# Performance work log

Hardware: AMD Instinct MI355X
Metric: run time of the kernel (lower is better)

## Reference

```python
import jax, jax.numpy as jnp
import numpy as np

B, N, D_IN = 4, 16384, 64          # batch, sequence (grid) length, model dim
H, DH = 8, 64                       # heads, dim per head
INNER = H * DH                      # 512


def setup_inputs() -> dict:
    key = jax.random.key(0)
    ks = jax.random.split(key, 7)
    s = 1.0 / np.sqrt(D_IN)
    return {
        "queries": jax.random.normal(ks[0], (B, N, D_IN), jnp.float32),
        "keys": jax.random.normal(ks[1], (B, N, D_IN), jnp.float32),
        "values": jax.random.normal(ks[2], (B, N, D_IN), jnp.float32),
        # torch nn.Linear weights are [out_features, in_features]
        "Wq": jax.random.normal(ks[3], (INNER, D_IN), jnp.float32) * s,
        "Wk": jax.random.normal(ks[4], (INNER, D_IN), jnp.float32) * s,
        "Wout": jax.random.normal(ks[5], (D_IN, INNER), jnp.float32) * (1.0 / np.sqrt(INNER)),
        "bout": jax.random.normal(ks[6], (D_IN,), jnp.float32) * 0.01,
    }


def reference(queries, keys, values, Wq, Wk, Wout, bout):
    b, n, _ = queries.shape
    # projections (NOTE: source uses to_k for values: values = self.to_k(values))
    q = (queries @ Wq.T).reshape(b, n, H, DH).transpose(0, 2, 1, 3)  # b h n d
    k = (keys    @ Wk.T).reshape(b, n, H, DH).transpose(0, 2, 1, 3)
    v = (values  @ Wk.T).reshape(b, n, H, DH).transpose(0, 2, 1, 3)
    # galerkin linear attention, associative form: (K^T V) first, then Q @ (.)
    # (the instance-norm outputs in the torch source are dead code on this path)
    dots = jnp.einsum('bhnd,bhne->bhde', k, v)            # [b,h,d,d]
    out = jnp.einsum('bhnd,bhde->bhne', q, dots) / n      # [b,h,n,d]
    out = out.transpose(0, 2, 1, 3).reshape(b, n, INNER)  # b n (h d)
    return out @ Wout.T + bout                             # [b,n,D_IN]
```

## Files before the change

kernel.cpp:

```cpp
#include <hip/hip_runtime.h>

#define NB 4
#define SEQ 16384
#define D 64
#define NH 8
#define INNER 512

constexpr int S_RPB  = 256;
constexpr int S_TILE = 32;

__global__ __launch_bounds__(256) void k_S(const float* __restrict__ keys,
                                           const float* __restrict__ values,
                                           float* __restrict__ S) {
    __shared__ float ks[S_TILE][D];
    __shared__ float vs[S_TILE][D];
    const int b = blockIdx.y;
    const int t = threadIdx.x;
    const size_t base = ((size_t)b * SEQ + (size_t)blockIdx.x * S_RPB) * D;
    const float4* ksrc = (const float4*)(keys + base);
    const float4* vsrc = (const float4*)(values + base);
    const int di = t >> 4;
    const int ej = t & 15;
    float acc[4][4] = {{0.f}};
    for (int tile = 0; tile < S_RPB / S_TILE; ++tile) {
        float4* kd = (float4*)&ks[0][0];
        float4* vd = (float4*)&vs[0][0];
        const int off = tile * (S_TILE * D / 4);
        kd[t]       = ksrc[off + t];
        kd[t + 256] = ksrc[off + t + 256];
        vd[t]       = vsrc[off + t];
        vd[t + 256] = vsrc[off + t + 256];
        __syncthreads();
        #pragma unroll 8
        for (int n = 0; n < S_TILE; ++n) {
            float kv[4], vv[4];
            #pragma unroll
            for (int a = 0; a < 4; ++a) kv[a] = ks[n][di + 16 * a];
            #pragma unroll
            for (int c = 0; c < 4; ++c) vv[c] = vs[n][ej + 16 * c];
            #pragma unroll
            for (int a = 0; a < 4; ++a)
                #pragma unroll
                for (int c = 0; c < 4; ++c)
                    acc[a][c] = fmaf(kv[a], vv[c], acc[a][c]);
        }
        __syncthreads();
    }
    float* Sb = S + b * D * D;
    #pragma unroll
    for (int a = 0; a < 4; ++a)
        #pragma unroll
        for (int c = 0; c < 4; ++c)
            atomicAdd(&Sb[(di + 16 * a) * D + (ej + 16 * c)], acc[a][c]);
}

__global__ __launch_bounds__(256) void k_G(const float* __restrict__ S,
                                           const float* __restrict__ Wq,
                                           const float* __restrict__ Wk,
                                           const float* __restrict__ Wout,
                                           float* __restrict__ G) {
    __shared__ float Ss[D][D];
    __shared__ float W1[D][D];
    __shared__ float T1[D][D];
    __shared__ float T2[D][D];
    const int b = blockIdx.x >> 3;
    const int h = blockIdx.x & 7;
    const int t = threadIdx.x;
    const int di = t >> 4, ej = t & 15;

    const float* Sb  = S + b * D * D;
    const float* Wkh = Wk + h * D * D;
    for (int i = t; i < D * D; i += 256) {
        (&Ss[0][0])[i] = Sb[i];
        (&W1[0][0])[i] = Wkh[i];
    }
    __syncthreads();

    float acc[4][4];

    #pragma unroll
    for (int a = 0; a < 4; ++a)
        #pragma unroll
        for (int c = 0; c < 4; ++c) acc[a][c] = 0.f;
    for (int i = 0; i < D; ++i) {
        float wa[4], sv[4];
        #pragma unroll
        for (int a = 0; a < 4; ++a) wa[a] = W1[di + 16 * a][i];
        #pragma unroll
        for (int c = 0; c < 4; ++c) sv[c] = Ss[i][ej + 16 * c];
        #pragma unroll
        for (int a = 0; a < 4; ++a)
            #pragma unroll
            for (int c = 0; c < 4; ++c) acc[a][c] = fmaf(wa[a], sv[c], acc[a][c]);
    }
    #pragma unroll
    for (int a = 0; a < 4; ++a)
        #pragma unroll
        for (int c = 0; c < 4; ++c) T1[di + 16 * a][ej + 16 * c] = acc[a][c];
    __syncthreads();

    #pragma unroll
    for (int a = 0; a < 4; ++a)
        #pragma unroll
        for (int c = 0; c < 4; ++c) acc[a][c] = 0.f;
    for (int i = 0; i < D; ++i) {
        float ta[4], wb[4];
        #pragma unroll
        for (int a = 0; a < 4; ++a) ta[a] = T1[di + 16 * a][i];
        #pragma unroll
        for (int c = 0; c < 4; ++c) wb[c] = W1[ej + 16 * c][i];
        #pragma unroll
        for (int a = 0; a < 4; ++a)
            #pragma unroll
            for (int c = 0; c < 4; ++c) acc[a][c] = fmaf(ta[a], wb[c], acc[a][c]);
    }
    #pragma unroll
    for (int a = 0; a < 4; ++a)
        #pragma unroll
        for (int c = 0; c < 4; ++c) T2[di + 16 * a][ej + 16 * c] = acc[a][c];
    __syncthreads();

    const float* Wqh = Wq + h * D * D;
    for (int i = t; i < D * D; i += 256) (&W1[0][0])[i] = Wqh[i];
    __syncthreads();

    #pragma unroll
    for (int a = 0; a < 4; ++a)
        #pragma unroll
        for (int c = 0; c < 4; ++c) acc[a][c] = 0.f;
    for (int i = 0; i < D; ++i) {
        float wa[4], tb[4];
        #pragma unroll
        for (int a = 0; a < 4; ++a) wa[a] = W1[i][di + 16 * a];
        #pragma unroll
        for (int c = 0; c < 4; ++c) tb[c] = T2[i][ej + 16 * c];
        #pragma unroll
        for (int a = 0; a < 4; ++a)
            #pragma unroll
            for (int c = 0; c < 4; ++c) acc[a][c] = fmaf(wa[a], tb[c], acc[a][c]);
    }
    #pragma unroll
    for (int a = 0; a < 4; ++a)
        #pragma unroll
        for (int c = 0; c < 4; ++c) T1[di + 16 * a][ej + 16 * c] = acc[a][c];
    __syncthreads();

    for (int i = t; i < D * D; i += 256) {
        int r = i >> 6, c2 = i & 63;
        (&W1[0][0])[i] = Wout[r * INNER + h * D + c2];
    }
    __syncthreads();

    #pragma unroll
    for (int a = 0; a < 4; ++a)
        #pragma unroll
        for (int c = 0; c < 4; ++c) acc[a][c] = 0.f;
    for (int i = 0; i < D; ++i) {
        float ta[4], wb[4];
        #pragma unroll
        for (int a = 0; a < 4; ++a) ta[a] = T1[di + 16 * a][i];
        #pragma unroll
        for (int c = 0; c < 4; ++c) wb[c] = W1[ej + 16 * c][i];
        #pragma unroll
        for (int a = 0; a < 4; ++a)
            #pragma unroll
            for (int c = 0; c < 4; ++c) acc[a][c] = fmaf(ta[a], wb[c], acc[a][c]);
    }
    const float invn = 1.0f / (float)SEQ;
    float* Gb = G + b * D * D;
    #pragma unroll
    for (int a = 0; a < 4; ++a)
        #pragma unroll
        for (int c = 0; c < 4; ++c)
            atomicAdd(&Gb[(di + 16 * a) * D + (ej + 16 * c)], acc[a][c] * invn);
}

constexpr int A_ROWS = 64;

__global__ __launch_bounds__(256) void k_apply(const float* __restrict__ queries,
                                               const float* __restrict__ G,
                                               const float* __restrict__ bout,
                                               float* __restrict__ out) {
    __shared__ float Gs[D][D];
    __shared__ float qs[A_ROWS][D + 4];
    const int b = blockIdx.y;
    const int t = threadIdx.x;
    const size_t base = ((size_t)b * SEQ + (size_t)blockIdx.x * A_ROWS) * D;
    const float4* qsrc = (const float4*)(queries + base);
    const float4* Gsrc = (const float4*)(G + b * D * D);
    float4* Gd = (float4*)&Gs[0][0];
    #pragma unroll
    for (int i = 0; i < 4; ++i) {
        const int idx = t + 256 * i;
        Gd[idx] = Gsrc[idx];
        float4 qv = qsrc[idx];
        const int r = idx >> 4;
        const int c = (idx & 15) * 4;
        *(float4*)&qs[r][c] = qv;
    }
    __syncthreads();

    const int d4 = (t & 15) * 4;
    const int rg = t >> 4;
    const float4 bo = *(const float4*)&bout[d4];
    float acc[4][4] = {{0.f}};
    #pragma unroll 8
    for (int i = 0; i < D; ++i) {
        const float4 g = *(const float4*)&Gs[i][d4];
        #pragma unroll
        for (int r = 0; r < 4; ++r) {
            const float qv = qs[rg + 16 * r][i];
            acc[r][0] = fmaf(qv, g.x, acc[r][0]);
            acc[r][1] = fmaf(qv, g.y, acc[r][1]);
            acc[r][2] = fmaf(qv, g.z, acc[r][2]);
            acc[r][3] = fmaf(qv, g.w, acc[r][3]);
        }
    }
    float* ob = out + base;
    #pragma unroll
    for (int r = 0; r < 4; ++r) {
        float4 o = make_float4(acc[r][0] + bo.x, acc[r][1] + bo.y,
                               acc[r][2] + bo.z, acc[r][3] + bo.w);
        *(float4*)&ob[(rg + 16 * r) * D + d4] = o;
    }
}

extern "C" void kernel_launch(void* const* d_in, const int* in_sizes, int n_in,
                              void* d_out, int out_size, void* d_ws, size_t ws_size,
                              hipStream_t stream) {
    const float* queries = (const float*)d_in[0];
    const float* keys    = (const float*)d_in[1];
    const float* values  = (const float*)d_in[2];
    const float* Wq      = (const float*)d_in[3];
    const float* Wk      = (const float*)d_in[4];
    const float* Wout    = (const float*)d_in[5];
    const float* bout    = (const float*)d_in[6];
    float* out = (float*)d_out;

    float* S = (float*)d_ws;
    float* G = S + NB * D * D;
    hipMemsetAsync(d_ws, 0, (size_t)2 * NB * D * D * sizeof(float), stream);

    k_S<<<dim3(SEQ / S_RPB, NB), 256, 0, stream>>>(keys, values, S);
    k_G<<<NB * NH, 256, 0, stream>>>(S, Wq, Wk, Wout, G);
    k_apply<<<dim3(SEQ / A_ROWS, NB), 256, 0, stream>>>(queries, G, bout, out);
}
```

Measured before the change: 152.5 us.

## Restructure pipeline into five kernels with weight-product precompute and atomic-free reduction

The three kernels are replaced by five. kA computes per-block partial K^T V tiles with no atomics and, in the same launch, the per-head weight products Wq^T Wk and Wout Wk. kB reduces the partials, and kC/kD fold the reduced matrix and the weight products into G using a different association, so only a small atomic reduction over head chunks remains. kE applies G to the queries using a transposed, XOR-swizzled copy of G in shared memory while reading queries straight from global memory. The aim is to remove the heavy atomic contention and the serial per-head matmul chain, at the cost of more launches and extra workspace traffic.

```diff
diff --git a/kernel.cpp b/kernel.cpp
--- a/kernel.cpp
+++ b/kernel.cpp
@@ -6,222 +6,253 @@
 #define NH 8
 #define INNER 512
 
-constexpr int S_RPB  = 256;
-constexpr int S_TILE = 32;
-
-__global__ __launch_bounds__(256) void k_S(const float* __restrict__ keys,
-                                           const float* __restrict__ values,
-                                           float* __restrict__ S) {
-    __shared__ float ks[S_TILE][D];
-    __shared__ float vs[S_TILE][D];
-    const int b = blockIdx.y;
-    const int t = threadIdx.x;
-    const size_t base = ((size_t)b * SEQ + (size_t)blockIdx.x * S_RPB) * D;
-    const float4* ksrc = (const float4*)(keys + base);
-    const float4* vsrc = (const float4*)(values + base);
-    const int di = t >> 4;
-    const int ej = t & 15;
-    float acc[4][4] = {{0.f}};
-    for (int tile = 0; tile < S_RPB / S_TILE; ++tile) {
-        float4* kd = (float4*)&ks[0][0];
-        float4* vd = (float4*)&vs[0][0];
-        const int off = tile * (S_TILE * D / 4);
-        kd[t]       = ksrc[off + t];
-        kd[t + 256] = ksrc[off + t + 256];
-        vd[t]       = vsrc[off + t];
-        vd[t + 256] = vsrc[off + t + 256];
-        __syncthreads();
-        #pragma unroll 8
-        for (int n = 0; n < S_TILE; ++n) {
-            float kv[4], vv[4];
-            #pragma unroll
-            for (int a = 0; a < 4; ++a) kv[a] = ks[n][di + 16 * a];
-            #pragma unroll
-            for (int c = 0; c < 4; ++c) vv[c] = vs[n][ej + 16 * c];
-            #pragma unroll
-            for (int a = 0; a < 4; ++a)
-                #pragma unroll
-                for (int c = 0; c < 4; ++c)
-                    acc[a][c] = fmaf(kv[a], vv[c], acc[a][c]);
-        }
-        __syncthreads();
-    }
-    float* Sb = S + b * D * D;
+typedef float f4 __attribute__((ext_vector_type(4)));
+
+#define OFF_PART 0
+#define OFF_S    (256 * 4096)
+#define OFF_P    (OFF_S + NB * 4096)
+#define OFF_Q    (OFF_P + 64 * INNER)
+#define OFF_XT   (OFF_Q + INNER * D)
+#define OFF_G    (OFF_XT + NB * 64 * INNER)
+
+__global__ __launch_bounds__(256) void kA(const float* __restrict__ keys,
+                                          const float* __restrict__ values,
+                                          const float* __restrict__ Wq,
+                                          const float* __restrict__ Wk,
+                                          const float* __restrict__ Wout,
+                                          float* __restrict__ ws) {
+    const int bid = blockIdx.x;
+    const int t = threadIdx.x;
+    const int w = t >> 6, l = t & 63;
+    const int dg = l >> 3, eg = l & 7;
+    const int dbase = (w & 1) * 32 + dg * 4;
+    const int ebase = (w >> 1) * 32 + eg * 4;
+
+    f4 acc[4];
+    #pragma unroll
+    for (int a = 0; a < 4; ++a) acc[a] = (f4)0.f;
+
+    if (bid < 256) {
+        const int b = bid >> 6;
+        const int row0 = (bid & 63) * 256;
+        const float* kp = keys   + ((size_t)b * SEQ + row0) * D;
+        const float* vp = values + ((size_t)b * SEQ + row0) * D;
+        #pragma unroll 4
+        for (int n = 0; n < 256; ++n) {
+            f4 kv = *(const f4*)(kp + n * D + dbase);
+            f4 vv = *(const f4*)(vp + n * D + ebase);
+            #pragma unroll
+            for (int a = 0; a < 4; ++a)
+                acc[a] += kv[a] * vv;
+        }
+        float* pp = ws + OFF_PART + (size_t)bid * 4096;
+        #pragma unroll
+        for (int a = 0; a < 4; ++a)
+            *(f4*)(pp + (dbase + a) * D + ebase) = acc[a];
+    } else if (bid < 264) {
+        const int h = bid - 256;
+        const float* wqp = Wq + (size_t)h * 64 * D;
+        const float* wkp = Wk + (size_t)h * 64 * D;
+        #pragma unroll 4
+        for (int i = 0; i < 64; ++i) {
+            f4 a4 = *(const f4*)(wqp + i * D + dbase);
+            f4 b4 = *(const f4*)(wkp + i * D + ebase);
+            #pragma unroll
+            for (int a = 0; a < 4; ++a)
+                acc[a] += a4[a] * b4;
+        }
+        float* pp = ws + OFF_P;
+        #pragma unroll
+        for (int a = 0; a < 4; ++a)
+            *(f4*)(pp + (dbase + a) * INNER + h * 64 + ebase) = acc[a];
+    } else {
+        const int h = bid - 264;
+        const float* wkp = Wk + (size_t)h * 64 * D;
+        #pragma unroll 2
+        for (int iq = 0; iq < 16; ++iq) {
+            f4 wo[4], wk4[4];
+            #pragma unroll
+            for (int a = 0; a < 4; ++a)
+                wo[a] = *(const f4*)(Wout + (size_t)(dbase + a) * INNER + h * 64 + iq * 4);
+            #pragma unroll
+            for (int ii = 0; ii < 4; ++ii)
+                wk4[ii] = *(const f4*)(wkp + (iq * 4 + ii) * D + ebase);
+            #pragma unroll
+            for (int a = 0; a < 4; ++a)
+                #pragma unroll
+                for (int ii = 0; ii < 4; ++ii)
+                    acc[a] += wo[a][ii] * wk4[ii];
+        }
+        float* qp = ws + OFF_Q;
+        #pragma unroll
+        for (int a = 0; a < 4; ++a)
+            *(f4*)(qp + (h * 64 + dbase + a) * D + ebase) = acc[a];
+    }
+}
+
+__global__ __launch_bounds__(256) void kB(float* __restrict__ ws) {
+    const int b = blockIdx.x >> 5;
+    const int seg = blockIdx.x & 31;
+    const int t = threadIdx.x;
+    const int el = seg * 128 + (t & 127);
+    const int half = t >> 7;
+    const float* pp = ws + OFF_PART + (size_t)b * 64 * 4096 + el;
+    float s = 0.f;
+    #pragma unroll 8
+    for (int p = 0; p < 32; ++p)
+        s += pp[(size_t)(half * 32 + p) * 4096];
+    __shared__ float red[256];
+    red[t] = s;
+    __syncthreads();
+    if (t < 128)
+        ws[OFF_S + b * 4096 + el] = red[t] + red[t + 128];
+}
+
+__global__ __launch_bounds__(256) void kC(float* __restrict__ ws) {
+    const int b = blockIdx.x >> 3, h = blockIdx.x & 7;
+    const int t = threadIdx.x;
+    if (h == 0) {
+        f4 z = (f4)0.f;
+        #pragma unroll
+        for (int m = 0; m < 4; ++m)
+            *(f4*)(ws + OFF_G + b * 4096 + t * 16 + m * 4) = z;
+    }
+    const int w = t >> 6, l = t & 63;
+    const int dbase = (w & 1) * 32 + (l >> 3) * 4;
+    const int ebase = (w >> 1) * 32 + (l & 7) * 4;
+    const float* Sp = ws + OFF_S + b * 4096;
+    const float* Qp = ws + OFF_Q + h * 64 * D;
+    float acc[4][4];
     #pragma unroll
     for (int a = 0; a < 4; ++a)
         #pragma unroll
+        for (int c = 0; c < 4; ++c) acc[a][c] = 0.f;
+    #pragma unroll 2
+    for (int iq = 0; iq < 16; ++iq) {
+        f4 s4[4], q4[4];
+        #pragma unroll
+        for (int a = 0; a < 4; ++a) s4[a] = *(const f4*)(Sp + (dbase + a) * D + iq * 4);
+        #pragma unroll
+        for (int c = 0; c < 4; ++c) q4[c] = *(const f4*)(Qp + (ebase + c) * D + iq * 4);
+        #pragma unroll
+        for (int a = 0; a < 4; ++a)
+            #pragma unroll
+            for (int c = 0; c < 4; ++c)
+                #pragma unroll
+                for (int ii = 0; ii < 4; ++ii)
+                    acc[a][c] = fmaf(s4[a][ii], q4[c][ii], acc[a][c]);
+    }
+    float* xp = ws + OFF_XT + (size_t)b * 64 * INNER;
+    #pragma unroll
+    for (int c = 0; c < 4; ++c) {
+        f4 o;
+        o[0] = acc[0][c]; o[1] = acc[1][c]; o[2] = acc[2][c]; o[3] = acc[3][c];
+        *(f4*)(xp + (size_t)(ebase + c) * INNER + h * 64 + dbase) = o;
+    }
+}
+
+__global__ __launch_bounds__(256) void kD(float* __restrict__ ws) {
+    const int b = blockIdx.x >> 4;
+    const int kc = (blockIdx.x & 15) * 32;
+    const int t = threadIdx.x;
+    const int w = t >> 6, l = t & 63;
+    const int dbase = (w & 1) * 32 + (l >> 3) * 4;
+    const int ebase = (w >> 1) * 32 + (l & 7) * 4;
+    const float* Pp = ws + OFF_P;
+    const float* Xp = ws + OFF_XT + (size_t)b * 64 * INNER;
+    float acc[4][4];
+    #pragma unroll
+    for (int a = 0; a < 4; ++a)
+        #pragma unroll
+        for (int c = 0; c < 4; ++c) acc[a][c] = 0.f;
+    #pragma unroll
+    for (int kq = 0; kq < 8; ++kq) {
+        f4 p4[4], x4[4];
+        #pragma unroll
+        for (int a = 0; a < 4; ++a) p4[a] = *(const f4*)(Pp + (size_t)(dbase + a) * INNER + kc + kq * 4);
+        #pragma unroll
+        for (int c = 0; c < 4; ++c) x4[c] = *(const f4*)(Xp + (size_t)(ebase + c) * INNER + kc + kq * 4);
+        #pragma unroll
+        for (int a = 0; a < 4; ++a)
+            #pragma unroll
+            for (int c = 0; c < 4; ++c)
+                #pragma unroll
+                for (int ii = 0; ii < 4; ++ii)
+                    acc[a][c] = fmaf(p4[a][ii], x4[c][ii], acc[a][c]);
+    }
+    const float invn = 1.0f / (float)SEQ;
+    float* Gp = ws + OFF_G + b * 4096;
+    #pragma unroll
+    for (int a = 0; a < 4; ++a)
+        #pragma unroll
         for (int c = 0; c < 4; ++c)
-            atomicAdd(&Sb[(di + 16 * a) * D + (ej + 16 * c)], acc[a][c]);
-}
-
-__global__ __launch_bounds__(256) void k_G(const float* __restrict__ S,
-                                           const float* __restrict__ Wq,
-                                           const float* __restrict__ Wk,
-                                           const float* __restrict__ Wout,
-                                           float* __restrict__ G) {
-    __shared__ float Ss[D][D];
-    __shared__ float W1[D][D];
-    __shared__ float T1[D][D];
-    __shared__ float T2[D][D];
-    const int b = blockIdx.x >> 3;
-    const int h = blockIdx.x & 7;
-    const int t = threadIdx.x;
-    const int di = t >> 4, ej = t & 15;
-
-    const float* Sb  = S + b * D * D;
-    const float* Wkh = Wk + h * D * D;
-    for (int i = t; i < D * D; i += 256) {
-        (&Ss[0][0])[i] = Sb[i];
-        (&W1[0][0])[i] = Wkh[i];
+            atomicAdd(&Gp[(dbase + a) * D + ebase + c], acc[a][c] * invn);
+}
+
+__global__ __launch_bounds__(256) void kE(const float* __restrict__ queries,
+                                          const float* __restrict__ bout,
+                                          const float* __restrict__ ws,
+                                          float* __restrict__ out) {
+    __shared__ float GTs[4096];
+    const int bid = blockIdx.x;
+    const int b = bid >> 6;
+    const int row0 = (bid & 63) * 256;
+    const int t = threadIdx.x;
+    {
+        const int d = t >> 2;
+        const int e0 = (t & 3) * 16;
+        #pragma unroll
+        for (int m4 = 0; m4 < 4; ++m4) {
+            f4 g = *(const f4*)(ws + OFF_G + b * 4096 + d * 64 + e0 + m4 * 4);
+            #pragma unroll
+            for (int mm = 0; mm < 4; ++mm) {
+                const int e = e0 + m4 * 4 + mm;
+                GTs[e * 64 + (((d >> 2) ^ ((e >> 3) & 7)) << 2) + (d & 3)] = g[mm];
+            }
+        }
     }
     __syncthreads();
 
-    float acc[4][4];
-
-    #pragma unroll
-    for (int a = 0; a < 4; ++a)
-        #pragma unroll
-        for (int c = 0; c < 4; ++c) acc[a][c] = 0.f;
-    for (int i = 0; i < D; ++i) {
-        float wa[4], sv[4];
-        #pragma unroll
-        for (int a = 0; a < 4; ++a) wa[a] = W1[di + 16 * a][i];
-        #pragma unroll
-        for (int c = 0; c < 4; ++c) sv[c] = Ss[i][ej + 16 * c];
-        #pragma unroll
-        for (int a = 0; a < 4; ++a)
-            #pragma unroll
-            for (int c = 0; c < 4; ++c) acc[a][c] = fmaf(wa[a], sv[c], acc[a][c]);
-    }
-    #pragma unroll
-    for (int a = 0; a < 4; ++a)
-        #pragma unroll
-        for (int c = 0; c < 4; ++c) T1[di + 16 * a][ej + 16 * c] = acc[a][c];
-    __syncthreads();
-
-    #pragma unroll
-    for (int a = 0; a < 4; ++a)
-        #pragma unroll
-        for (int c = 0; c < 4; ++c) acc[a][c] = 0.f;
-    for (int i = 0; i < D; ++i) {
-        float ta[4], wb[4];
-        #pragma unroll
-        for (int a = 0; a < 4; ++a) ta[a] = T1[di + 16 * a][i];
-        #pragma unroll
-        for (int c = 0; c < 4; ++c) wb[c] = W1[ej + 16 * c][i];
-        #pragma unroll
-        for (int a = 0; a < 4; ++a)
-            #pragma unroll
-            for (int c = 0; c < 4; ++c) acc[a][c] = fmaf(ta[a], wb[c], acc[a][c]);
-    }
-    #pragma unroll
-    for (int a = 0; a < 4; ++a)
-        #pragma unroll
-        for (int c = 0; c < 4; ++c) T2[di + 16 * a][ej + 16 * c] = acc[a][c];
-    __syncthreads();
-
-    const float* Wqh = Wq + h * D * D;
-    for (int i = t; i < D * D; i += 256) (&W1[0][0])[i] = Wqh[i];
-    __syncthreads();
-
-    #pragma unroll
-    for (int a = 0; a < 4; ++a)
-        #pragma unroll
-        for (int c = 0; c < 4; ++c) acc[a][c] = 0.f;
-    for (int i = 0; i < D; ++i) {
-        float wa[4], tb[4];
-        #pragma unroll
-        for (int a = 0; a < 4; ++a) wa[a] = W1[i][di + 16 * a];
-        #pragma unroll
-        for (int c = 0; c < 4; ++c) tb[c] = T2[i][ej + 16 * c];
-        #pragma unroll
-        for (int a = 0; a < 4; ++a)
-            #pragma unroll
-            for (int c = 0; c < 4; ++c) acc[a][c] = fmaf(wa[a], tb[c], acc[a][c]);
-    }
-    #pragma unroll
-    for (int a = 0; a < 4; ++a)
-        #pragma unroll
-        for (int c = 0; c < 4; ++c) T1[di + 16 * a][ej + 16 * c] = acc[a][c];
-    __syncthreads();
-
-    for (int i = t; i < D * D; i += 256) {
-        int r = i >> 6, c2 = i & 63;
-        (&W1[0][0])[i] = Wout[r * INNER + h * D + c2];
-    }
-    __syncthreads();
-
-    #pragma unroll
-    for (int a = 0; a < 4; ++a)
-        #pragma unroll
-        for (int c = 0; c < 4; ++c) acc[a][c] = 0.f;
-    for (int i = 0; i < D; ++i) {
-        float ta[4], wb[4];
-        #pragma unroll
-        for (int a = 0; a < 4; ++a) ta[a] = T1[di + 16 * a][i];
-        #pragma unroll
-        for (int c = 0; c < 4; ++c) wb[c] = W1[ej + 16 * c][i];
-        #pragma unroll
-        for (int a = 0; a < 4; ++a)
-            #pragma unroll
-            for (int c = 0; c < 4; ++c) acc[a][c] = fmaf(ta[a], wb[c], acc[a][c]);
-    }
-    const float invn = 1.0f / (float)SEQ;
-    float* Gb = G + b * D * D;
-    #pragma unroll
-    for (int a = 0; a < 4; ++a)
-        #pragma unroll
-        for (int c = 0; c < 4; ++c)
-            atomicAdd(&Gb[(di + 16 * a) * D + (ej + 16 * c)], acc[a][c] * invn);
-}
-
-constexpr int A_ROWS = 64;
-
-__global__ __launch_bounds__(256) void k_apply(const float* __restrict__ queries,
-                                               const float* __restrict__ G,
-                                               const float* __restrict__ bout,
-                                               float* __restrict__ out) {
-    __shared__ float Gs[D][D];
-    __shared__ float qs[A_ROWS][D + 4];
-    const int b = blockIdx.y;
-    const int t = threadIdx.x;
-    const size_t base = ((size_t)b * SEQ + (size_t)blockIdx.x * A_ROWS) * D;
-    const float4* qsrc = (const float4*)(queries + base);
-    const float4* Gsrc = (const float4*)(G + b * D * D);
-    float4* Gd = (float4*)&Gs[0][0];
-    #pragma unroll
-    for (int i = 0; i < 4; ++i) {
-        const int idx = t + 256 * i;
-        Gd[idx] = Gsrc[idx];
-        float4 qv = qsrc[idx];
-        const int r = idx >> 4;
-        const int c = (idx & 15) * 4;
-        *(float4*)&qs[r][c] = qv;
-    }
-    __syncthreads();
-
-    const int d4 = (t & 15) * 4;
-    const int rg = t >> 4;
-    const float4 bo = *(const float4*)&bout[d4];
-    float acc[4][4] = {{0.f}};
-    #pragma unroll 8
-    for (int i = 0; i < D; ++i) {
-        const float4 g = *(const float4*)&Gs[i][d4];
+    const int w = t >> 6, l = t & 63;
+    const int ng = l >> 3, eg = l & 7;
+    const f4 bo0 = *(const f4*)(bout + eg * 8);
+    const f4 bo1 = *(const f4*)(bout + eg * 8 + 4);
+    const float* qp = queries + ((size_t)b * SEQ + row0 + w * 64) * D;
+    float* op = out + ((size_t)b * SEQ + row0 + w * 64) * D;
+
+    #pragma unroll
+    for (int sub = 0; sub < 2; ++sub) {
+        const float* qs = qp + (sub * 32 + ng * 4) * D;
+        f4 acc[4][2];
+        #pragma unroll
+        for (int r = 0; r < 4; ++r) { acc[r][0] = (f4)0.f; acc[r][1] = (f4)0.f; }
+        #pragma unroll 4
+        for (int dq = 0; dq < 16; ++dq) {
+            f4 q4[4], g4[8];
+            #pragma unroll
+            for (int r = 0; r < 4; ++r)
+                q4[r] = *(const f4*)(qs + r * D + dq * 4);
+            #pragma unroll
+            for (int c = 0; c < 8; ++c) {
+                const int e = eg * 8 + c;
+                g4[c] = *(const f4*)&GTs[e * 64 + ((dq ^ eg) << 2)];
+            }
+            #pragma unroll
+            for (int r = 0; r < 4; ++r)
+                #pragma unroll
+                for (int c = 0; c < 8; ++c)
+                    #pragma unroll
+                    for (int ii = 0; ii < 4; ++ii)
+                        acc[r][c >> 2][c & 3] = fmaf(q4[r][ii], g4[c][ii], acc[r][c >> 2][c & 3]);
+        }
         #pragma unroll
         for (int r = 0; r < 4; ++r) {
-            const float qv = qs[rg + 16 * r][i];
-            acc[r][0] = fmaf(qv, g.x, acc[r][0]);
-            acc[r][1] = fmaf(qv, g.y, acc[r][1]);
-            acc[r][2] = fmaf(qv, g.z, acc[r][2]);
-            acc[r][3] = fmaf(qv, g.w, acc[r][3]);
-        }
-    }
-    float* ob = out + base;
-    #pragma unroll
-    for (int r = 0; r < 4; ++r) {
-        float4 o = make_float4(acc[r][0] + bo.x, acc[r][1] + bo.y,
-                               acc[r][2] + bo.z, acc[r][3] + bo.w);
-        *(float4*)&ob[(rg + 16 * r) * D + d4] = o;
+            const int row = (sub * 32 + ng * 4 + r) * D;
+            f4 o0 = acc[r][0] + bo0;
+            f4 o1 = acc[r][1] + bo1;
+            *(f4*)(op + row + eg * 8) = o0;
+            *(f4*)(op + row + eg * 8 + 4) = o1;
+        }
     }
 }
 
@@ -235,13 +266,11 @@
     const float* Wk      = (const float*)d_in[4];
     const float* Wout    = (const float*)d_in[5];
     const float* bout    = (const float*)d_in[6];
-    float* out = (float*)d_out;
-
-    float* S = (float*)d_ws;
-    float* G = S + NB * D * D;
-    hipMemsetAsync(d_ws, 0, (size_t)2 * NB * D * D * sizeof(float), stream);
-
-    k_S<<<dim3(SEQ / S_RPB, NB), 256, 0, stream>>>(keys, values, S);
-    k_G<<<NB * NH, 256, 0, stream>>>(S, Wq, Wk, Wout, G);
-    k_apply<<<dim3(SEQ / A_ROWS, NB), 256, 0, stream>>>(queries, G, bout, out);
-}
+    float* ws = (float*)d_ws;
+
+    kA<<<272, 256, 0, stream>>>(keys, values, Wq, Wk, Wout, ws);
+    kB<<<128, 256, 0, stream>>>(ws);
+    kC<<<32,  256, 0, stream>>>(ws);
+    kD<<<64,  256, 0, stream>>>(ws);
+    kE<<<256, 256, 0, stream>>>(queries, bout, ws, (float*)d_out);
+}
```

New measurement: 158.4 us. 3.9% more time.
